# Kernel optimization log

Measured on AMD Instinct MI355X. Metric: run time of the kernel, lower is better.

## Reference

```python
import jax, jax.numpy as jnp
import numpy as np

B, S, H, D = 16, 512, 12, 64          # batch, seq, heads, head_dim
HID = H * D                            # 768
MAX_POS = 512
CHAR_HP = 0.5
WORD_HP = 0.5


def setup_inputs() -> dict:
    key = jax.random.key(0)
    ks = jax.random.split(key, 12)
    s = 0.02
    return {
        "hidden_states": jax.random.normal(ks[0], (B, S, HID), jnp.float32),
        "attention_mask": jnp.zeros((B, 1, 1, S), jnp.float32),
        "character_level_matrix": jax.random.randint(ks[1], (B, S, S), 0, 8),
        "word_level_matrix": jax.random.randint(ks[2], (B, S, S), 0, 8),
        "Wq": jax.random.normal(ks[3], (HID, HID), jnp.float32) * s,
        "bq": jnp.zeros((HID,), jnp.float32),
        "Wk": jax.random.normal(ks[4], (HID, HID), jnp.float32) * s,
        "bk": jnp.zeros((HID,), jnp.float32),
        "Wv": jax.random.normal(ks[5], (HID, HID), jnp.float32) * s,
        "bv": jnp.zeros((HID,), jnp.float32),
        "dist_emb": jax.random.normal(ks[6], (2 * MAX_POS - 1, D), jnp.float32) * s,
        "char_emb": jax.random.normal(ks[7], (8, 1), jnp.float32) * s,
        "word_emb": jax.random.normal(ks[8], (8, 1), jnp.float32) * s,
    }


def reference(hidden_states, attention_mask, character_level_matrix,
              word_level_matrix, Wq, bq, Wk, bk, Wv, bv,
              dist_emb, char_emb, word_emb):
    # level nn-embedding lookup: [B,S,S] int -> [B,S,S] float
    char_bias = char_emb[character_level_matrix][..., 0]
    word_bias = word_emb[word_level_matrix][..., 0]

    def heads(x):  # [B,S,HID] -> [B,H,S,D]
        return x.reshape(B, S, H, D).transpose(0, 2, 1, 3)

    q = heads(hidden_states @ Wq.T + bq)
    k = heads(hidden_states @ Wk.T + bk)
    v = heads(hidden_states @ Wv.T + bv)

    scores = jnp.einsum('bhld,bhrd->bhlr', q, k)
    # level biases broadcast over heads
    scores = scores + CHAR_HP * char_bias[:, None] + WORD_HP * word_bias[:, None]

    # relative_key_query positional scores
    pos = jnp.arange(S)
    distance = pos[:, None] - pos[None, :]
    pe = dist_emb[distance + MAX_POS - 1]  # [S(l), S(r), D]
    scores = scores + jnp.einsum('bhld,lrd->bhlr', q, pe) \
                    + jnp.einsum('bhrd,lrd->bhlr', k, pe)

    scores = scores / jnp.sqrt(jnp.float32(D)) + attention_mask
    probs = jax.nn.softmax(scores, axis=-1)
    ctx = jnp.einsum('bhlr,bhrd->bhld', probs, v)
    return ctx.transpose(0, 2, 1, 3).reshape(B, S, HID)
```

## Files before the change

### kernel.cpp

```cpp
#include <hip/hip_runtime.h>
#include <stdint.h>

#define Bv 16
#define Sv 512
#define Hv 12
#define Dv 64
#define HIDv 768

typedef __attribute__((ext_vector_type(8))) short bf8_t;
typedef __attribute__((ext_vector_type(4))) float f32x4;
typedef __attribute__((ext_vector_type(8))) unsigned short u16x8;
typedef __attribute__((ext_vector_type(4))) unsigned short u16x4;

__device__ __forceinline__ float b2f(unsigned short u){
    union { unsigned int i; float f; } x; x.i = ((unsigned int)u) << 16; return x.f;
}
__device__ __forceinline__ unsigned short f2b(float f){
    union { float f; unsigned int i; } x; x.f = f;
    unsigned int r = x.i + 0x7fff + ((x.i >> 16) & 1);
    return (unsigned short)(r >> 16);
}
__device__ __forceinline__ void gload16(const unsigned short* g, unsigned short* l){
    __builtin_amdgcn_global_load_lds(
        (const __attribute__((address_space(1))) void*)g,
        (__attribute__((address_space(3))) void*)l, 16, 0, 0);
}

#define RS 0.18033688f
#define LOG2E 1.44269504f

__global__ void cvt_bf16(const float* __restrict__ src, unsigned short* __restrict__ dst, int n4){
    int i = blockIdx.x * 256 + threadIdx.x;
    int stride = gridDim.x * 256;
    for (; i < n4; i += stride){
        float4 v = ((const float4*)src)[i];
        u16x4 o = { f2b(v.x), f2b(v.y), f2b(v.z), f2b(v.w) };
        ((u16x4*)dst)[i] = o;
    }
}

__global__ void cvt_w3(const float* __restrict__ a, const float* __restrict__ b,
                       const float* __restrict__ c, unsigned short* __restrict__ dst, int n4each){
    int i = blockIdx.x * 256 + threadIdx.x;
    if (i >= 3*n4each) return;
    int which = i / n4each, j = i - which*n4each;
    const float* src = which == 0 ? a : (which == 1 ? b : c);
    float4 v = ((const float4*)src)[j];
    u16x4 o = { f2b(v.x), f2b(v.y), f2b(v.z), f2b(v.w) };
    ((u16x4*)dst)[i] = o;
}

__global__ __launch_bounds__(256) void prep_bias_t(
    const int* __restrict__ cmat, const int* __restrict__ wmat,
    const float* __restrict__ mask, const float* __restrict__ ce, const float* __restrict__ we,
    unsigned short* __restrict__ lvlt)
{
    __shared__ float tab[64];
    __shared__ float mrow[64];
    const int t = threadIdx.x;
    const int blk = blockIdx.x;
    const int c8 = blk & 7, lt = (blk >> 3) & 7, b = blk >> 6;
    if (t < 64) tab[t] = (0.5f*ce[t>>3] + 0.5f*we[t&7]) * RS;
    if (t >= 64 && t < 128) mrow[t-64] = mask[b*512 + c8*64 + (t-64)] * LOG2E;
    __syncthreads();
    const int w = t >> 6, lane = t & 63, g = lane >> 4, cc = lane & 15;
    const int llb = lt*64 + w*16 + g*4;
    const int rlb = c8*64 + cc;
    unsigned short o[16];
    #pragma unroll
    for (int reg = 0; reg < 4; ++reg){
        const int* cr = cmat + ((size_t)b*512 + llb + reg)*512 + rlb;
        const int* wr = wmat + ((size_t)b*512 + llb + reg)*512 + rlb;
        #pragma unroll
        for (int i = 0; i < 4; ++i){
            int cv = cr[i*16], wv = wr[i*16];
            o[reg*4 + i] = f2b(tab[(cv<<3)|wv] + mrow[i*16 + cc]);
        }
    }
    unsigned short* dst = lvlt + ((size_t)blk*256 + t)*16;
    *(u16x8*)dst       = *(u16x8*)&o[0];
    *(u16x8*)(dst + 8) = *(u16x8*)&o[8];
}

__global__ __launch_bounds__(256,3) void qkv_gemm(
    const unsigned short* __restrict__ Xb,
    const unsigned short* __restrict__ Wb,
    const float* __restrict__ bq, const float* __restrict__ bk, const float* __restrict__ bv,
    unsigned short* __restrict__ qkb,
    unsigned short* __restrict__ vtb)
{
    __shared__ unsigned short Ab[128*40];
    __shared__ unsigned short Bb[128*40];
    const int t = threadIdx.x;
    const int w = t >> 6, lane = t & 63, g = lane >> 4, cc = lane & 15;
    const int wm = w >> 1, wn = w & 1;
    const int m0 = blockIdx.x * 128;
    const int n0 = blockIdx.y * 128;

    const f32x4 fz = {0.f,0.f,0.f,0.f};
    f32x4 acc[4][4];
    #pragma unroll
    for (int i = 0; i < 4; ++i)
        #pragma unroll
        for (int j = 0; j < 4; ++j) acc[i][j] = fz;

    u16x8 pa[2], pb[2];
    #pragma unroll
    for (int r = 0; r < 2; ++r){
        int chunk = t + r*256; int row = chunk >> 2; int ch = chunk & 3;
        pa[r] = *(const u16x8*)(Xb + (size_t)(m0+row)*768 + ch*8);
        pb[r] = *(const u16x8*)(Wb + (size_t)(n0+row)*768 + ch*8);
    }
    for (int k0 = 0; k0 < 768; k0 += 32){
        __syncthreads();
        #pragma unroll
        for (int r = 0; r < 2; ++r){
            int chunk = t + r*256; int row = chunk >> 2; int ch = chunk & 3;
            *(u16x8*)&Ab[row*40 + ch*8] = pa[r];
            *(u16x8*)&Bb[row*40 + ch*8] = pb[r];
        }
        __syncthreads();
        if (k0 + 32 < 768){
            #pragma unroll
            for (int r = 0; r < 2; ++r){
                int chunk = t + r*256; int row = chunk >> 2; int ch = chunk & 3;
                pa[r] = *(const u16x8*)(Xb + (size_t)(m0+row)*768 + (k0+32) + ch*8);
                pb[r] = *(const u16x8*)(Wb + (size_t)(n0+row)*768 + (k0+32) + ch*8);
            }
        }
        bf8_t af[4], bfr[4];
        #pragma unroll
        for (int mf = 0; mf < 4; ++mf)
            af[mf] = *(const bf8_t*)&Ab[(wm*64 + mf*16 + cc)*40 + g*8];
        #pragma unroll
        for (int nf = 0; nf < 4; ++nf)
            bfr[nf] = *(const bf8_t*)&Bb[(wn*64 + nf*16 + cc)*40 + g*8];
        #pragma unroll
        for (int mf = 0; mf < 4; ++mf)
            #pragma unroll
            for (int nf = 0; nf < 4; ++nf)
                acc[mf][nf] = __builtin_amdgcn_mfma_f32_16x16x32_bf16(af[mf], bfr[nf], acc[mf][nf], 0,0,0);
    }

    const int b  = m0 >> 9;
    const int s0 = (m0 & 511) + wm*64;
    const int nbase = n0 + wn*64;
    const int proj = nbase / 768;
    const int nin0 = nbase % 768;
    const float* bias = proj == 0 ? bq : (proj == 1 ? bk : bv);
    #pragma unroll
    for (int nf = 0; nf < 4; ++nf){
        int nin = nin0 + nf*16 + cc;
        int h = nin >> 6, d = nin & 63;
        float bvv = bias[nin];
        #pragma unroll
        for (int mf = 0; mf < 4; ++mf){
            int s = s0 + mf*16 + g*4;
            if (proj < 2){
                unsigned short* base = qkb + (((((size_t)proj*Bv + b)*Hv + h)*Sv + s)*Dv + d);
                #pragma unroll
                for (int r2 = 0; r2 < 4; ++r2)
                    base[(size_t)r2*Dv] = f2b(acc[mf][nf][r2] + bvv);
            } else {
                u16x4 o = { f2b(acc[mf][nf][0]+bvv), f2b(acc[mf][nf][1]+bvv),
                            f2b(acc[mf][nf][2]+bvv), f2b(acc[mf][nf][3]+bvv) };
                *(u16x4*)(vtb + ((((size_t)b*Hv + h)*Dv + d)*Sv + s)) = o;
            }
        }
    }
}

__global__ __launch_bounds__(256,2) void attn(
    const unsigned short* __restrict__ qkb,
    const unsigned short* __restrict__ vtb,
    const unsigned short* __restrict__ deb,
    const unsigned short* __restrict__ lvlt,
    float* __restrict__ out)
{
    __shared__ __align__(16) unsigned short sm[37504];
    unsigned short* ks   = sm;
    unsigned short* vsq  = sm + 4096;
    unsigned short* des  = sm + 8192;
    float*          t1c  = (float*)(sm + 16384);
    float*          t2c  = (float*)(sm + 24832);
    unsigned short* P    = sm + 33408;

    const int t = threadIdx.x, w = t >> 6, lane = t & 63, g = lane >> 4, cc = lane & 15;
    const int lr8 = lane >> 3, lc8 = lane & 7;

    const int wg = blockIdx.x;
    const int xcd = wg & 7, inner = wg >> 3;
    const int b  = ((inner & 1) << 3) | xcd;
    const int r2 = inner >> 1;
    const int h  = r2 % 12, lt = r2 / 12;
    const int l0 = lt * 64;

    const unsigned short* qp = qkb + ((((size_t)0*Bv + b)*Hv + h)*Sv + l0)*Dv;
    const unsigned short* kp = qkb + ((((size_t)1*Bv + b)*Hv + h)*Sv)*Dv;
    const unsigned short* vp = vtb + (((size_t)b*Hv + h)*Dv)*Sv;
    const unsigned short* lvbase = lvlt + (((size_t)b*8 + lt)*8)*256*16 + (size_t)t*16;

    const f32x4 fz = {0.f,0.f,0.f,0.f};
    const int llb = w*16 + g*4;

    auto stage_k = [&](int r0){
        #pragma unroll
        for (int j = 0; j < 2; ++j){
            int row = w*16 + j*8 + lr8;
            int ch  = lc8 ^ (row & 7);
            gload16(kp + (size_t)(r0 + row)*64 + ch*8, ks + w*1024 + j*512);
        }
    };
    auto stage_de = [&](int r0){
        const int base = l0 - r0 + 448;
        #pragma unroll
        for (int j = 0; j < 4; ++j){
            int row = w*32 + j*8 + lr8;
            int gr = base + row; if (gr > 1022) gr = 1022; if (gr < 0) gr = 0;
            int ch  = lc8 ^ (row & 7);
            gload16(deb + (size_t)gr*64 + ch*8, des + w*2048 + j*512);
        }
    };
    auto stage_v = [&](int r0){
        #pragma unroll
        for (int j = 0; j < 2; ++j){
            int row = w*16 + j*8 + lr8;
            int ch  = lc8 ^ (row & 7);
            gload16(vp + (size_t)row*512 + r0 + ch*8, vsq + w*1024 + j*512);
        }
    };

    bf8_t qf0, qf1;
    {
        int qrow = w*16 + cc;
        qf0 = *(const bf8_t*)(qp + (size_t)qrow*64 + g*8);
        qf1 = *(const bf8_t*)(qp + (size_t)qrow*64 + (g+4)*8);
    }
    stage_k(0); stage_de(0); stage_v(0);
    __syncthreads();

    float l_run[4] = {0.f,0.f,0.f,0.f};
    f32x4 ctx[4] = {fz,fz,fz,fz};

    for (int c8 = 0; c8 < 8; ++c8){
        const int r0 = c8 * 64;
        u16x8 lva = *(const u16x8*)(lvbase + (size_t)c8*256*16);
        u16x8 lvb = *(const u16x8*)(lvbase + (size_t)c8*256*16 + 8);

        __builtin_amdgcn_s_setprio(1);
        f32x4 accs[4];
        bf8_t kf0, kf1;
        #pragma unroll
        for (int i = 0; i < 4; ++i){
            int row = i*16 + cc;
            bf8_t b0 = *(const bf8_t*)&ks[row*64 + ((g       ^ (row & 7))*8)];
            bf8_t b1 = *(const bf8_t*)&ks[row*64 + (((g + 4) ^ (row & 7))*8)];
            if (i == w){ kf0 = b0; kf1 = b1; }
            f32x4 a = fz;
            a = __builtin_amdgcn_mfma_f32_16x16x32_bf16(qf0, b0, a, 0,0,0);
            a = __builtin_amdgcn_mfma_f32_16x16x32_bf16(qf1, b1, a, 0,0,0);
            accs[i] = a;
        }
        #pragma unroll
        for (int i = 0; i < 5; ++i){
            int jb = (w + i)*16 + cc;
            bf8_t d0 = *(const bf8_t*)&des[jb*64 + ((g       ^ (jb & 7))*8)];
            bf8_t d1 = *(const bf8_t*)&des[jb*64 + (((g + 4) ^ (jb & 7))*8)];
            f32x4 a = fz;
            a = __builtin_amdgcn_mfma_f32_16x16x32_bf16(qf0, d0, a, 0,0,0);
            a = __builtin_amdgcn_mfma_f32_16x16x32_bf16(qf1, d1, a, 0,0,0);
            #pragma unroll
            for (int reg = 0; reg < 4; ++reg){
                int ll = llb + reg;
                int rl = ll + 63 - jb;
                if (rl >= 0 && rl < 64) t1c[ll*66 + rl] = a[reg];
            }
        }
        #pragma unroll
        for (int i = 0; i < 5; ++i){
            int jb = (3 - w + i)*16 + cc;
            bf8_t d0 = *(const bf8_t*)&des[jb*64 + ((g       ^ (jb & 7))*8)];
            bf8_t d1 = *(const bf8_t*)&des[jb*64 + (((g + 4) ^ (jb & 7))*8)];
            f32x4 a = fz;
            a = __builtin_amdgcn_mfma_f32_16x16x32_bf16(kf0, d0, a, 0,0,0);
            a = __builtin_amdgcn_mfma_f32_16x16x32_bf16(kf1, d1, a, 0,0,0);
            #pragma unroll
            for (int reg = 0; reg < 4; ++reg){
                int rl = llb + reg;
                int ll = rl + jb - 63;
                if (ll >= 0 && ll < 64) t2c[rl*67 + ll] = a[reg];
            }
        }
        __builtin_amdgcn_s_setprio(0);
        __syncthreads();

        if (c8 < 7){ stage_k(r0 + 64); stage_de(r0 + 64); }

        float t1v[4][4], t2v[4][4];
        {
            const float* t1b = t1c + llb*66 + cc;
            #pragma unroll
            for (int reg = 0; reg < 4; ++reg)
                #pragma unroll
                for (int i = 0; i < 4; ++i)
                    t1v[reg][i] = t1b[reg*66 + i*16];
            const float* t2b = t2c + cc*67 + llb;
            #pragma unroll
            for (int i = 0; i < 4; ++i)
                #pragma unroll
                for (int reg = 0; reg < 4; ++reg)
                    t2v[reg][i] = t2b[i*1072 + reg];
        }
        #pragma unroll
        for (int reg = 0; reg < 4; ++reg){
            int ll = llb + reg;
            float ps = 0.f;
            #pragma unroll
            for (int i = 0; i < 4; ++i){
                float lvv = b2f(reg < 2 ? (unsigned short)lva[reg*4 + i]
                                        : (unsigned short)lvb[(reg-2)*4 + i]);
                float sv = (accs[i][reg] + t1v[reg][i] + t2v[reg][i]) * RS + lvv;
                float p = __builtin_amdgcn_exp2f(sv);
                ps += p;
                int rl = i*16 + cc;
                P[ll*64 + (((rl >> 3) ^ (ll & 7)) << 3) + (rl & 7)] = f2b(p);
            }
            ps += __shfl_xor(ps, 1); ps += __shfl_xor(ps, 2);
            ps += __shfl_xor(ps, 4); ps += __shfl_xor(ps, 8);
            l_run[reg] += ps;
        }

        __builtin_amdgcn_s_setprio(1);
        #pragma unroll
        for (int kh = 0; kh < 2; ++kh){
            int prow = w*16 + cc;
            bf8_t pf = *(const bf8_t*)&P[prow*64 + (((g + 4*kh) ^ (prow & 7)) << 3)];
            #pragma unroll
            for (int nf = 0; nf < 4; ++nf){
                int vr = nf*16 + cc;
                bf8_t vf = *(const bf8_t*)&vsq[vr*64 + (((g + 4*kh) ^ (vr & 7))*8)];
                ctx[nf] = __builtin_amdgcn_mfma_f32_16x16x32_bf16(pf, vf, ctx[nf], 0,0,0);
            }
        }
        __builtin_amdgcn_s_setprio(0);

        if (c8 < 7){
            __syncthreads();
            stage_v(r0 + 64);
            __syncthreads();
        }
    }

    #pragma unroll
    for (int nf = 0; nf < 4; ++nf){
        #pragma unroll
        for (int reg = 0; reg < 4; ++reg){
            int ll = llb + reg;
            out[((size_t)b*Sv + l0 + ll)*HIDv + h*64 + nf*16 + cc] = ctx[nf][reg] / l_run[reg];
        }
    }
}

extern "C" void kernel_launch(void* const* d_in, const int* in_sizes, int n_in,
                              void* d_out, int out_size, void* d_ws, size_t ws_size,
                              hipStream_t stream)
{
    const float* hs   = (const float*)d_in[0];
    const float* mask = (const float*)d_in[1];
    const int*   cmat = (const int*)  d_in[2];
    const int*   wmat = (const int*)  d_in[3];
    const float* Wq   = (const float*)d_in[4];
    const float* bq   = (const float*)d_in[5];
    const float* Wk   = (const float*)d_in[6];
    const float* bk   = (const float*)d_in[7];
    const float* Wv   = (const float*)d_in[8];
    const float* bv   = (const float*)d_in[9];
    const float* de   = (const float*)d_in[10];
    const float* ce   = (const float*)d_in[11];
    const float* we   = (const float*)d_in[12];
    float* out = (float*)d_out;

    unsigned short* Xb   = (unsigned short*)d_ws;
    unsigned short* Wb   = Xb   + 6291456;
    unsigned short* deb  = Wb   + 1769472;
    unsigned short* qkb  = deb  + 65536;
    unsigned short* vtb  = qkb  + 12582912;
    unsigned short* lvlt = vtb  + 6291456;

    cvt_bf16<<<2048, 256, 0, stream>>>(hs, Xb, 1572864);
    cvt_w3<<<1728, 256, 0, stream>>>(Wq, Wk, Wv, Wb, 147456);
    cvt_bf16<<<64,   256, 0, stream>>>(de, deb, 16368);
    prep_bias_t<<<1024, 256, 0, stream>>>(cmat, wmat, mask, ce, we, lvlt);

    qkv_gemm<<<dim3(64, 18), 256, 0, stream>>>(Xb, Wb, bq, bk, bv, qkb, vtb);
    attn<<<1536, 256, 0, stream>>>(qkb, vtb, deb, lvlt, out);
}
```

Baseline: 157.3 us.

## Read distance embeddings directly from global and shrink LDS footprint

Drops LDS staging of the distance-embedding rows and loads the embedding fragments straight from global/L2 into registers. The q·pe and k·pe MFMA passes now share one loop over the same fragments. The second bias buffer is stored as bf16, and both bias buffers are laid out transposed so the softmax stage can read them with vector loads. This cuts LDS use from about 75KB to about 50KB and removes a global-to-LDS copy per tile, but adds uncached-in-LDS global loads inside the compute loop and bf16 rounding of one positional term.

```diff
diff --git a/kernel.cpp b/kernel.cpp
--- a/kernel.cpp
+++ b/kernel.cpp
@@ -177,13 +177,12 @@
     const unsigned short* __restrict__ lvlt,
     float* __restrict__ out)
 {
-    __shared__ __align__(16) unsigned short sm[37504];
-    unsigned short* ks   = sm;
-    unsigned short* vsq  = sm + 4096;
-    unsigned short* des  = sm + 8192;
-    float*          t1c  = (float*)(sm + 16384);
-    float*          t2c  = (float*)(sm + 24832);
-    unsigned short* P    = sm + 33408;
+    __shared__ __align__(16) unsigned short sm[25344];
+    unsigned short* ks  = sm;
+    unsigned short* vsq = sm + 4096;
+    unsigned short* P   = sm + 8192;
+    float*          t1c = (float*)(sm + 12288);
+    unsigned short* t2c = sm + 20992;
 
     const int t = threadIdx.x, w = t >> 6, lane = t & 63, g = lane >> 4, cc = lane & 15;
     const int lr8 = lane >> 3, lc8 = lane & 7;
@@ -202,6 +201,8 @@
 
     const f32x4 fz = {0.f,0.f,0.f,0.f};
     const int llb = w*16 + g*4;
+    const int R   = 3 - w;
+    const int rl2b = R*16 + g*4;
 
     auto stage_k = [&](int r0){
         #pragma unroll
@@ -209,16 +210,6 @@
             int row = w*16 + j*8 + lr8;
             int ch  = lc8 ^ (row & 7);
             gload16(kp + (size_t)(r0 + row)*64 + ch*8, ks + w*1024 + j*512);
-        }
-    };
-    auto stage_de = [&](int r0){
-        const int base = l0 - r0 + 448;
-        #pragma unroll
-        for (int j = 0; j < 4; ++j){
-            int row = w*32 + j*8 + lr8;
-            int gr = base + row; if (gr > 1022) gr = 1022; if (gr < 0) gr = 0;
-            int ch  = lc8 ^ (row & 7);
-            gload16(deb + (size_t)gr*64 + ch*8, des + w*2048 + j*512);
         }
     };
     auto stage_v = [&](int r0){
@@ -236,7 +227,7 @@
         qf0 = *(const bf8_t*)(qp + (size_t)qrow*64 + g*8);
         qf1 = *(const bf8_t*)(qp + (size_t)qrow*64 + (g+4)*8);
     }
-    stage_k(0); stage_de(0); stage_v(0);
+    stage_k(0); stage_v(0);
     __syncthreads();
 
     float l_run[4] = {0.f,0.f,0.f,0.f};
@@ -244,6 +235,8 @@
 
     for (int c8 = 0; c8 < 8; ++c8){
         const int r0 = c8 * 64;
+        const int base = l0 - r0 + 448;
+
         u16x8 lva = *(const u16x8*)(lvbase + (size_t)c8*256*16);
         u16x8 lvb = *(const u16x8*)(lvbase + (size_t)c8*256*16 + 8);
 
@@ -255,7 +248,7 @@
             int row = i*16 + cc;
             bf8_t b0 = *(const bf8_t*)&ks[row*64 + ((g       ^ (row & 7))*8)];
             bf8_t b1 = *(const bf8_t*)&ks[row*64 + (((g + 4) ^ (row & 7))*8)];
-            if (i == w){ kf0 = b0; kf1 = b1; }
+            if (i == R){ kf0 = b0; kf1 = b1; }
             f32x4 a = fz;
             a = __builtin_amdgcn_mfma_f32_16x16x32_bf16(qf0, b0, a, 0,0,0);
             a = __builtin_amdgcn_mfma_f32_16x16x32_bf16(qf1, b1, a, 0,0,0);
@@ -263,53 +256,33 @@
         }
         #pragma unroll
         for (int i = 0; i < 5; ++i){
-            int jb = (w + i)*16 + cc;
-            bf8_t d0 = *(const bf8_t*)&des[jb*64 + ((g       ^ (jb & 7))*8)];
-            bf8_t d1 = *(const bf8_t*)&des[jb*64 + (((g + 4) ^ (jb & 7))*8)];
-            f32x4 a = fz;
-            a = __builtin_amdgcn_mfma_f32_16x16x32_bf16(qf0, d0, a, 0,0,0);
-            a = __builtin_amdgcn_mfma_f32_16x16x32_bf16(qf1, d1, a, 0,0,0);
+            int jrow = base + (w + i)*16 + cc;
+            bf8_t d0 = *(const bf8_t*)(deb + (size_t)jrow*64 + g*8);
+            bf8_t d1 = *(const bf8_t*)(deb + (size_t)jrow*64 + (g+4)*8);
+            f32x4 a1 = fz, a2 = fz;
+            a1 = __builtin_amdgcn_mfma_f32_16x16x32_bf16(qf0, d0, a1, 0,0,0);
+            a1 = __builtin_amdgcn_mfma_f32_16x16x32_bf16(qf1, d1, a1, 0,0,0);
+            a2 = __builtin_amdgcn_mfma_f32_16x16x32_bf16(kf0, d0, a2, 0,0,0);
+            a2 = __builtin_amdgcn_mfma_f32_16x16x32_bf16(kf1, d1, a2, 0,0,0);
             #pragma unroll
             for (int reg = 0; reg < 4; ++reg){
-                int ll = llb + reg;
-                int rl = ll + 63 - jb;
-                if (rl >= 0 && rl < 64) t1c[ll*66 + rl] = a[reg];
-            }
-        }
-        #pragma unroll
-        for (int i = 0; i < 5; ++i){
-            int jb = (3 - w + i)*16 + cc;
-            bf8_t d0 = *(const bf8_t*)&des[jb*64 + ((g       ^ (jb & 7))*8)];
-            bf8_t d1 = *(const bf8_t*)&des[jb*64 + (((g + 4) ^ (jb & 7))*8)];
-            f32x4 a = fz;
-            a = __builtin_amdgcn_mfma_f32_16x16x32_bf16(kf0, d0, a, 0,0,0);
-            a = __builtin_amdgcn_mfma_f32_16x16x32_bf16(kf1, d1, a, 0,0,0);
-            #pragma unroll
-            for (int reg = 0; reg < 4; ++reg){
-                int rl = llb + reg;
-                int ll = rl + jb - 63;
-                if (ll >= 0 && ll < 64) t2c[rl*67 + ll] = a[reg];
+                int rl1 = 4*g + reg - 16*i - cc + 63;
+                if (rl1 >= 0 && rl1 < 64) t1c[rl1*68 + llb + reg] = a1[reg];
+                int ll2 = 4*g + reg + 16*i + cc - 15;
+                if (ll2 >= 0 && ll2 < 64) t2c[(rl2b + reg)*68 + ll2] = f2b(a2[reg]);
             }
         }
         __builtin_amdgcn_s_setprio(0);
         __syncthreads();
 
-        if (c8 < 7){ stage_k(r0 + 64); stage_de(r0 + 64); }
-
-        float t1v[4][4], t2v[4][4];
-        {
-            const float* t1b = t1c + llb*66 + cc;
-            #pragma unroll
-            for (int reg = 0; reg < 4; ++reg)
-                #pragma unroll
-                for (int i = 0; i < 4; ++i)
-                    t1v[reg][i] = t1b[reg*66 + i*16];
-            const float* t2b = t2c + cc*67 + llb;
-            #pragma unroll
-            for (int i = 0; i < 4; ++i)
-                #pragma unroll
-                for (int reg = 0; reg < 4; ++reg)
-                    t2v[reg][i] = t2b[i*1072 + reg];
+        if (c8 < 7) stage_k(r0 + 64);
+
+        f32x4 t1v4[4];
+        u16x4 t2v4[4];
+        #pragma unroll
+        for (int i = 0; i < 4; ++i){
+            t1v4[i] = *(const f32x4*)&t1c[(16*i + cc)*68 + llb];
+            t2v4[i] = *(const u16x4*)&t2c[(16*i + cc)*68 + llb];
         }
         #pragma unroll
         for (int reg = 0; reg < 4; ++reg){
@@ -319,7 +292,7 @@
             for (int i = 0; i < 4; ++i){
                 float lvv = b2f(reg < 2 ? (unsigned short)lva[reg*4 + i]
                                         : (unsigned short)lvb[(reg-2)*4 + i]);
-                float sv = (accs[i][reg] + t1v[reg][i] + t2v[reg][i]) * RS + lvv;
+                float sv = (accs[i][reg] + t1v4[i][reg] + b2f((unsigned short)t2v4[i][reg])) * RS + lvv;
                 float p = __builtin_amdgcn_exp2f(sv);
                 ps += p;
                 int rl = i*16 + cc;
```

After: 171.8 us. +9.2%, slower.
